# Performance work log

Measured on AMD Instinct MI355X. Metric: run time of the kernel, lower is better.

The kernel has to match this reference:

```python
import jax, jax.numpy as jnp
import numpy as np

N = 100000      # nodes
E = 1600000     # edges
R = 4           # relations
F = 128         # node feature dim
EMB = 128       # embedding size
HID = 256       # hidden size
B = 1024        # number of (nest, food) queries


def setup_inputs() -> dict:
    key = jax.random.key(0)
    ks = jax.random.split(key, 12)
    s1 = 1.0 / np.sqrt(F)
    s2 = 1.0 / np.sqrt(EMB)
    sf = 1.0 / np.sqrt(2 * EMB)
    return {
        "x": jax.random.normal(ks[0], (N, F), jnp.float32),
        "edge_index": jax.random.randint(ks[1], (2, E), 0, N),
        "edge_type": jax.random.randint(ks[2], (E,), 0, R),
        "nest_idx": jax.random.randint(ks[3], (B,), 0, N),
        "food_idx": jax.random.randint(ks[4], (B,), 0, N),
        "W_rel1": jax.random.normal(ks[5], (R, F, EMB), jnp.float32) * s1,
        "W_root1": jax.random.normal(ks[6], (F, EMB), jnp.float32) * s1,
        "b1": jnp.zeros((EMB,), jnp.float32),
        "W_rel2": jax.random.normal(ks[7], (R, EMB, EMB), jnp.float32) * s2,
        "W_root2": jax.random.normal(ks[8], (EMB, EMB), jnp.float32) * s2,
        "b2": jnp.zeros((EMB,), jnp.float32),
        "W_fc": jax.random.normal(ks[9], (2 * EMB, HID), jnp.float32) * sf,
        "b_fc": jnp.zeros((HID,), jnp.float32),
    }


def rgcn_conv(x, src, dst, etype, W_rel, W_root, b):
    # Per-relation transform of all nodes: [N, R, O]
    h = jnp.einsum('nf,rfo->nro', x, W_rel)
    msgs = h[src, etype]                      # [E, O] gather per edge
    # Mean aggregation per (dst, relation), PyG RGCNConv default
    key = dst * R + etype                     # [E]
    deg = jax.ops.segment_sum(jnp.ones((E,), x.dtype), key, num_segments=N * R)
    norm = 1.0 / jnp.maximum(deg, 1.0)
    out = jax.ops.segment_sum(msgs * norm[key][:, None], dst, num_segments=N)
    return out + x @ W_root + b


def reference(x, edge_index, edge_type, nest_idx, food_idx,
              W_rel1, W_root1, b1, W_rel2, W_root2, b2, W_fc, b_fc):
    src, dst = edge_index[0], edge_index[1]
    h = jax.nn.relu(rgcn_conv(x, src, dst, edge_type, W_rel1, W_root1, b1))
    h = rgcn_conv(h, src, dst, edge_type, W_rel2, W_root2, b2)
    combined = jnp.concatenate([h[nest_idx], h[food_idx]], axis=-1)  # [B, 2*EMB]
    return jax.nn.relu(combined @ W_fc + b_fc)                        # [B, HID]
```

## Files before the change

kernel.cpp:

```cpp
#include <hip/hip_runtime.h>
#include <stdint.h>

#define NN 100000
#define NE 1600000
#define NR 4
#define FD 128
#define KA 512
#define KT 640
#define NQ 1024
#define HIDN 256

#define MPAD 100096
#define NCHK (MPAD / 128)
#define NBE ((NE + 2047) / 2048)
#define NCHB ((NN + 255) / 256)
#define MAXS 49152
#define NCH1 (MAXS / 256)
#define MAXL2 65536

using u16 = unsigned short;
using u32 = unsigned int;
using u8 = unsigned char;
typedef __attribute__((ext_vector_type(8))) __bf16 bf16x8;
typedef __attribute__((ext_vector_type(4))) float f32x4;

__device__ __forceinline__ u16 f2b(float f) {
    u32 u = __builtin_bit_cast(u32, f);
    u32 r = u + 0x7FFFu + ((u >> 16) & 1u);
    return (u16)(r >> 16);
}
__device__ __forceinline__ float b2f_lo(u32 v) { return __builtin_bit_cast(float, v << 16); }
__device__ __forceinline__ float b2f_hi(u32 v) { return __builtin_bit_cast(float, v & 0xFFFF0000u); }
__device__ __forceinline__ u32 pack2(float a, float b) {
    return (u32)f2b(a) | ((u32)f2b(b) << 16);
}
__device__ __forceinline__ void gload_lds16(const void* g, void* l) {
    __builtin_amdgcn_global_load_lds((const __attribute__((address_space(1))) u32*)g,
                                     (__attribute__((address_space(3))) u32*)l, 16, 0, 0);
}

__global__ __launch_bounds__(256) void mark_T(const int* __restrict__ nest,
                                              const int* __restrict__ food,
                                              u8* __restrict__ bmT, u8* __restrict__ bmS) {
    int i = blockIdx.x * 256 + threadIdx.x;
    if (i < NQ)          { int q = nest[i];      bmT[q] = 1; bmS[q] = 1; }
    else if (i < 2 * NQ) { int q = food[i - NQ]; bmT[q] = 1; bmS[q] = 1; }
}

__global__ __launch_bounds__(256) void filter_l2(const int* __restrict__ ei,
                                                 const int* __restrict__ et,
                                                 const u8* __restrict__ bmT,
                                                 u8* __restrict__ bmS,
                                                 int* __restrict__ cnts,
                                                 u32* __restrict__ l2a,
                                                 u32* __restrict__ l2d) {
    __shared__ int lcnt, lbase;
    __shared__ u32 ba[2048], bd[2048];
    int t = threadIdx.x;
    if (t == 0) lcnt = 0;
    __syncthreads();
    int e0 = blockIdx.x * 2048;
    for (int j = 0; j < 8; ++j) {
        int e = e0 + j * 256 + t;
        if (e < NE) {
            int dst = ei[NE + e];
            if (bmT[dst]) {
                int src = ei[e];
                int r = et[e];
                int pos = atomicAdd(&lcnt, 1);
                ba[pos] = (u32)src | ((u32)r << 17);
                bd[pos] = (u32)dst;
                bmS[src] = 1;
            }
        }
    }
    __syncthreads();
    if (t == 0) lbase = atomicAdd(&cnts[2], lcnt);
    __syncthreads();
    for (int i = t; i < lcnt; i += 256) {
        l2a[lbase + i] = ba[i];
        l2d[lbase + i] = bd[i];
    }
}

__global__ __launch_bounds__(256) void bm_chunk(const u8* __restrict__ bmS,
                                                const u8* __restrict__ bmT,
                                                int* __restrict__ cS, int* __restrict__ cT) {
    __shared__ int sS[256], sT[256];
    int b = blockIdx.x, t = threadIdx.x;
    int n = b * 256 + t;
    int vs = (n < NN) ? bmS[n] : 0;
    int vt = (n < NN) ? bmT[n] : 0;
    sS[t] = vs; sT[t] = vt;
    __syncthreads();
    for (int o = 128; o > 0; o >>= 1) {
        if (t < o) { sS[t] += sS[t + o]; sT[t] += sT[t + o]; }
        __syncthreads();
    }
    if (t == 0) { cS[b] = sS[0]; cT[b] = sT[0]; }
}

__global__ __launch_bounds__(512) void bm_scan(const int* __restrict__ cS,
                                               const int* __restrict__ cT,
                                               int* __restrict__ oS, int* __restrict__ oT,
                                               int* __restrict__ cnts) {
    __shared__ int sS[512], sT[512];
    int t = threadIdx.x;
    int vs = (t < NCHB) ? cS[t] : 0;
    int vt = (t < NCHB) ? cT[t] : 0;
    sS[t] = vs; sT[t] = vt;
    __syncthreads();
    for (int o = 1; o < 512; o <<= 1) {
        int a = (t >= o) ? sS[t - o] : 0;
        int c = (t >= o) ? sT[t - o] : 0;
        __syncthreads();
        sS[t] += a; sT[t] += c;
        __syncthreads();
    }
    if (t < NCHB) { oS[t] = sS[t] - vs; oT[t] = sT[t] - vt; }
    if (t == NCHB - 1) { cnts[0] = sS[t]; cnts[1] = sT[t]; }
}

__global__ __launch_bounds__(256) void bm_write(const u8* __restrict__ bmS,
                                                const u8* __restrict__ bmT,
                                                const int* __restrict__ oS,
                                                const int* __restrict__ oT,
                                                int* __restrict__ sid, int* __restrict__ tidm,
                                                int* __restrict__ snode) {
    __shared__ int sS[256], sT[256];
    int b = blockIdx.x, t = threadIdx.x;
    int n = b * 256 + t;
    int vs = (n < NN) ? bmS[n] : 0;
    int vt = (n < NN) ? bmT[n] : 0;
    sS[t] = vs; sT[t] = vt;
    __syncthreads();
    for (int o = 1; o < 256; o <<= 1) {
        int a = (t >= o) ? sS[t - o] : 0;
        int c = (t >= o) ? sT[t - o] : 0;
        __syncthreads();
        sS[t] += a; sT[t] += c;
        __syncthreads();
    }
    if (n < NN) {
        int is = oS[b] + sS[t] - vs;
        int it = oT[b] + sT[t] - vt;
        sid[n] = is;
        tidm[n] = it;
        if (vs) snode[is] = n;
    }
}

__global__ __launch_bounds__(256) void l2_count(const int* __restrict__ cnts,
                                                const u32* __restrict__ l2a,
                                                const u32* __restrict__ l2d,
                                                const int* __restrict__ tidm,
                                                int* __restrict__ deg2) {
    int n = cnts[2];
    for (int i = blockIdx.x * 256 + threadIdx.x; i < n; i += gridDim.x * 256)
        atomicAdd(&deg2[tidm[l2d[i]] * 4 + ((l2a[i] >> 17) & 3)], 1);
}

__global__ __launch_bounds__(1024) void l2_scan(const int* __restrict__ deg2,
                                                int* __restrict__ offs2,
                                                int* __restrict__ cur2) {
    __shared__ int sm[1024];
    int t = threadIdx.x;
    int v[8];
    int s = 0;
    for (int j = 0; j < 8; ++j) { v[j] = deg2[t * 8 + j]; s += v[j]; }
    sm[t] = s;
    __syncthreads();
    for (int o = 1; o < 1024; o <<= 1) {
        int n = (t >= o) ? sm[t - o] : 0;
        __syncthreads();
        sm[t] += n;
        __syncthreads();
    }
    int ex = sm[t] - s;
    for (int j = 0; j < 8; ++j) { offs2[t * 8 + j] = ex; cur2[t * 8 + j] = ex; ex += v[j]; }
    if (t == 1023) offs2[8192] = ex;
}

__global__ __launch_bounds__(256) void l2_scatter(const int* __restrict__ cnts,
                                                  const u32* __restrict__ l2a,
                                                  const u32* __restrict__ l2d,
                                                  const int* __restrict__ tidm,
                                                  const int* __restrict__ sid,
                                                  int* __restrict__ cur2,
                                                  int* __restrict__ spack2) {
    int n = cnts[2];
    for (int i = blockIdx.x * 256 + threadIdx.x; i < n; i += gridDim.x * 256) {
        u32 a = l2a[i];
        int k = tidm[l2d[i]] * 4 + ((a >> 17) & 3);
        int pos = atomicAdd(&cur2[k], 1);
        spack2[pos] = sid[a & 0x1FFFFu];
    }
}

__global__ __launch_bounds__(256) void l1_count(const int* __restrict__ ei,
                                                const int* __restrict__ et,
                                                const u8* __restrict__ bmS,
                                                const int* __restrict__ sid,
                                                int* __restrict__ deg1) {
    int e0 = blockIdx.x * 2048;
    int t = threadIdx.x;
    for (int j = 0; j < 8; ++j) {
        int e = e0 + j * 256 + t;
        if (e < NE) {
            int dst = ei[NE + e];
            if (bmS[dst]) atomicAdd(&deg1[sid[dst] * 4 + et[e]], 1);
        }
    }
}

__global__ __launch_bounds__(256) void l1_chunk(const int* __restrict__ deg1,
                                                int* __restrict__ c1) {
    __shared__ int sm[256];
    int b = blockIdx.x, t = threadIdx.x;
    int n = b * 256 + t;
    int s = deg1[4 * n] + deg1[4 * n + 1] + deg1[4 * n + 2] + deg1[4 * n + 3];
    sm[t] = (s + 7) & ~7;
    __syncthreads();
    for (int o = 128; o > 0; o >>= 1) {
        if (t < o) sm[t] += sm[t + o];
        __syncthreads();
    }
    if (t == 0) c1[b] = sm[0];
}

__global__ __launch_bounds__(256) void l1_scan(const int* __restrict__ c1,
                                               int* __restrict__ o1) {
    __shared__ int sm[256];
    int t = threadIdx.x;
    int v = (t < NCH1) ? c1[t] : 0;
    sm[t] = v;
    __syncthreads();
    for (int o = 1; o < 256; o <<= 1) {
        int n = (t >= o) ? sm[t - o] : 0;
        __syncthreads();
        sm[t] += n;
        __syncthreads();
    }
    if (t < NCH1) o1[t] = sm[t] - v;
}

__global__ __launch_bounds__(256) void l1_write(const int* __restrict__ deg1,
                                                const int* __restrict__ o1,
                                                int* __restrict__ offs6s,
                                                int* __restrict__ cur1,
                                                int* __restrict__ spack1) {
    __shared__ int sm[256];
    int b = blockIdx.x, t = threadIdx.x;
    int n = b * 256 + t;
    int d0 = deg1[4 * n], d1 = deg1[4 * n + 1], d2 = deg1[4 * n + 2], d3 = deg1[4 * n + 3];
    int s = d0 + d1 + d2 + d3;
    int sp = (s + 7) & ~7;
    sm[t] = sp;
    __syncthreads();
    for (int o = 1; o < 256; o <<= 1) {
        int v = (t >= o) ? sm[t - o] : 0;
        __syncthreads();
        sm[t] += v;
        __syncthreads();
    }
    int e0 = o1[b] + sm[t] - sp;
    int e1 = e0 + d0, e2 = e1 + d1, e3 = e2 + d2, e4 = e3 + d3, eL = e0 + sp;
    int* o6 = offs6s + (size_t)n * 6;
    o6[0] = e0; o6[1] = e1; o6[2] = e2; o6[3] = e3; o6[4] = e4; o6[5] = eL;
    cur1[4 * n] = e0; cur1[4 * n + 1] = e1; cur1[4 * n + 2] = e2; cur1[4 * n + 3] = e3;
    for (int i = e4; i < eL; ++i) spack1[i] = 5 * NN;
}

__global__ __launch_bounds__(256) void l1_scatter(const int* __restrict__ ei,
                                                  const int* __restrict__ et,
                                                  const u8* __restrict__ bmS,
                                                  const int* __restrict__ sid,
                                                  int* __restrict__ cur1,
                                                  int* __restrict__ spack1) {
    int e0 = blockIdx.x * 2048;
    int t = threadIdx.x;
    for (int j = 0; j < 8; ++j) {
        int e = e0 + j * 256 + t;
        if (e < NE) {
            int dst = ei[NE + e];
            if (bmS[dst]) {
                int r = et[e];
                int src = ei[e];
                int pos = atomicAdd(&cur1[sid[dst] * 4 + r], 1);
                spack1[pos] = r * NN + src;
            }
        }
    }
}

__global__ __launch_bounds__(256) void cvt_bf16(const float* __restrict__ in,
                                                u16* __restrict__ outp, int n) {
    int i = blockIdx.x * 256 + threadIdx.x;
    int idx = i * 4;
    if (idx >= n) return;
    float4 v = *(const float4*)(in + idx);
    u32 lo = (u32)f2b(v.x) | ((u32)f2b(v.y) << 16);
    u32 hi = (u32)f2b(v.z) | ((u32)f2b(v.w) << 16);
    *(uint2*)(outp + idx) = make_uint2(lo, hi);
}

__global__ __launch_bounds__(256) void prep_B5(const float* __restrict__ Wrel,
                                               const float* __restrict__ Wroot,
                                               u16* __restrict__ Bt5) {
    int i = blockIdx.x * 256 + threadIdx.x;
    if (i >= 5 * FD * FD) return;
    int tb = i / (FD * FD);
    int rem = i - tb * (FD * FD);
    int o = rem / FD;
    int k = rem - o * FD;
    float v = (tb < 4) ? Wrel[(size_t)tb * FD * FD + (size_t)k * FD + o]
                       : Wroot[(size_t)k * FD + o];
    Bt5[i] = f2b(v);
}

__global__ __launch_bounds__(256) void prep_B(const float* __restrict__ Wrel,
                                              const float* __restrict__ Wroot,
                                              u16* __restrict__ Bt) {
    int i = blockIdx.x * 256 + threadIdx.x;
    if (i >= FD * KT) return;
    int k = i % KT;
    int o = i / KT;
    float v = (k < 512) ? Wrel[(size_t)k * FD + o] : Wroot[(size_t)(k - 512) * FD + o];
    Bt[i] = f2b(v);
}

__global__ __launch_bounds__(256) void gemm_y(const u16* __restrict__ X,
                                              const u16* __restrict__ Bt5,
                                              u16* __restrict__ Y) {
    __shared__ u16 As[2][8192];
    int blk = blockIdx.x;
    int rel = blk / NCHK;
    int chunk = blk - rel * NCHK;
    int row0 = chunk * 128;
    int tid = threadIdx.x;
    int wid = tid >> 6, lane = tid & 63;
    int wm = wid >> 1, wn = wid & 1;
    int lr = lane & 15, hi = lane >> 4;
    const u16* Btr = Bt5 + (size_t)rel * FD * FD;
    u16* C = Y + (size_t)rel * NN * FD;

    int srow = wid * 8 + (lane >> 3);
    int sg = (lane & 7) ^ ((lane >> 3) & 7);
#pragma unroll
    for (int s = 0; s < 2; ++s)
#pragma unroll
        for (int i = 0; i < 4; ++i) {
            int r = i * 32 + srow;
            int gr = row0 + r;
            gload_lds16(X + (size_t)gr * FD + s * 64 + sg * 8,
                        (char*)As[s] + i * 4096 + wid * 1024);
        }
    __syncthreads();

    f32x4 acc[4][4];
#pragma unroll
    for (int i = 0; i < 4; ++i)
#pragma unroll
        for (int j = 0; j < 4; ++j) acc[i][j] = (f32x4){0.f, 0.f, 0.f, 0.f};

#pragma unroll
    for (int t = 0; t < 2; ++t) {
#pragma unroll
        for (int kk = 0; kk < 2; ++kk) {
            bf16x8 bfr[4], afr[4];
#pragma unroll
            for (int ni = 0; ni < 4; ++ni) {
                int col = wn * 64 + ni * 16 + lr;
                bfr[ni] = *reinterpret_cast<const bf16x8*>(
                    Btr + (size_t)col * FD + t * 64 + kk * 32 + hi * 8);
            }
#pragma unroll
            for (int mi = 0; mi < 4; ++mi) {
                int r = wm * 64 + mi * 16 + lr;
                int sp = (kk * 4 + hi) ^ (r & 7);
                afr[mi] = *reinterpret_cast<const bf16x8*>((char*)As[t] + r * 128 + sp * 16);
            }
#pragma unroll
            for (int mi = 0; mi < 4; ++mi)
#pragma unroll
                for (int ni = 0; ni < 4; ++ni)
                    acc[mi][ni] = __builtin_amdgcn_mfma_f32_16x16x32_bf16(afr[mi], bfr[ni], acc[mi][ni], 0, 0, 0);
        }
    }
#pragma unroll
    for (int mi = 0; mi < 4; ++mi)
#pragma unroll
        for (int ni = 0; ni < 4; ++ni) {
            int col = wn * 64 + ni * 16 + lr;
#pragma unroll
            for (int rg = 0; rg < 4; ++rg) {
                int row = row0 + wm * 64 + mi * 16 + hi * 4 + rg;
                if (row < NN) C[(size_t)row * FD + col] = f2b(acc[mi][ni][rg]);
            }
        }
}

__global__ __launch_bounds__(256) void agg_s(const int* __restrict__ cnts,
                                             const int* __restrict__ offs6s,
                                             const int* __restrict__ spack1,
                                             const int* __restrict__ snode,
                                             const u32* __restrict__ Y,
                                             const float* __restrict__ bias,
                                             u16* __restrict__ h1s) {
    int wid = threadIdx.x >> 6, lane = threadIdx.x & 63;
    int row = blockIdx.x * 4 + wid;
    if (row >= cnts[0]) return;

    const int* ob = offs6s + (size_t)row * 6;
    int o0 = __builtin_amdgcn_readfirstlane(ob[0]);
    int o1 = __builtin_amdgcn_readfirstlane(ob[1]);
    int o2 = __builtin_amdgcn_readfirstlane(ob[2]);
    int o3 = __builtin_amdgcn_readfirstlane(ob[3]);
    int o4 = __builtin_amdgcn_readfirstlane(ob[4]);
    int oL = __builtin_amdgcn_readfirstlane(ob[5]);

    float a00 = 0, a01 = 0, a10 = 0, a11 = 0, a20 = 0, a21 = 0, a30 = 0, a31 = 0;

    for (int e = o0; e < oL; e += 8) {
        int p[8];
        u32 v[8];
#pragma unroll
        for (int j = 0; j < 8; ++j)
            p[j] = __builtin_amdgcn_readfirstlane(spack1[e + j]);
#pragma unroll
        for (int j = 0; j < 8; ++j) v[j] = Y[(size_t)p[j] * 64 + lane];
#pragma unroll
        for (int j = 0; j < 8; ++j) {
            int ij = e + j;
            float f0 = b2f_lo(v[j]);
            float f1 = b2f_hi(v[j]);
            if (ij < o1)      { a00 += f0; a01 += f1; }
            else if (ij < o2) { a10 += f0; a11 += f1; }
            else if (ij < o3) { a20 += f0; a21 += f1; }
            else              { a30 += f0; a31 += f1; }
        }
    }

    int d0 = o1 - o0, d1 = o2 - o1, d2 = o3 - o2, d3 = o4 - o3;
    float s0 = 1.0f / (float)(d0 > 1 ? d0 : 1);
    float s1 = 1.0f / (float)(d1 > 1 ? d1 : 1);
    float s2 = 1.0f / (float)(d2 > 1 ? d2 : 1);
    float s3 = 1.0f / (float)(d3 > 1 ? d3 : 1);
    float sum0 = a00 * s0 + a10 * s1 + a20 * s2 + a30 * s3;
    float sum1 = a01 * s0 + a11 * s1 + a21 * s2 + a31 * s3;
    int node = __builtin_amdgcn_readfirstlane(snode[row]);
    u32 rv = Y[((size_t)4 * NN + node) * 64 + lane];
    float2 bb = *reinterpret_cast<const float2*>(bias + lane * 2);
    float r0 = fmaxf(sum0 + b2f_lo(rv) + bb.x, 0.f);
    float r1 = fmaxf(sum1 + b2f_hi(rv) + bb.y, 0.f);
    *(u32*)(h1s + (size_t)row * FD + lane * 2) = pack2(r0, r1);
}

__global__ __launch_bounds__(256) void agg_q2(const int* __restrict__ offs2,
                                              const int* __restrict__ spack2,
                                              const u32* __restrict__ h1s4,
                                              const int* __restrict__ nest,
                                              const int* __restrict__ food,
                                              const int* __restrict__ tidm,
                                              const int* __restrict__ sid,
                                              u16* __restrict__ Aout,
                                              int* __restrict__ sidq) {
    int wid = threadIdx.x >> 6, lane = threadIdx.x & 63;
    int row = blockIdx.x * 4 + wid;
    if (row >= 2 * NQ) return;
    int q = (row < NQ) ? nest[row] : food[row - NQ];
    q = __builtin_amdgcn_readfirstlane(q);
    int tq = __builtin_amdgcn_readfirstlane(tidm[q]);
    if (lane == 0) sidq[row] = sid[q];
    const int* ob = offs2 + (size_t)tq * 4;
    int o[5];
#pragma unroll
    for (int i = 0; i < 5; ++i) o[i] = __builtin_amdgcn_readfirstlane(ob[i]);
    u16* Ao = Aout + (size_t)row * KA + lane * 2;
#pragma unroll
    for (int r = 0; r < 4; ++r) {
        int s = o[r], t = o[r + 1], last = t - 1;
        float a0 = 0, a1 = 0;
        for (int e = s; e < t; e += 8) {
            int p[8];
            u32 v[8];
#pragma unroll
            for (int j = 0; j < 8; ++j) {
                int ij = e + j;
                int cl = ij <= last ? ij : last;
                int pv = __builtin_amdgcn_readfirstlane(spack2[cl]);
                p[j] = (ij <= last) ? pv : MAXS;
            }
#pragma unroll
            for (int j = 0; j < 8; ++j) v[j] = h1s4[(size_t)p[j] * 64 + lane];
#pragma unroll
            for (int j = 0; j < 8; ++j) { a0 += b2f_lo(v[j]); a1 += b2f_hi(v[j]); }
        }
        int d = t - s;
        float sc = 1.0f / (float)(d > 1 ? d : 1);
        *(u32*)(Ao + r * 128) = pack2(a0 * sc, a1 * sc);
    }
}

__global__ __launch_bounds__(256) void gemm_lds3(const u16* __restrict__ A,
                                                 const u16* __restrict__ rootSrc,
                                                 const int* __restrict__ rootIdx,
                                                 const u16* __restrict__ Bt,
                                                 const float* __restrict__ bias,
                                                 float* __restrict__ Cout, int M) {
    __shared__ u16 As[3][8192];
    int tid = threadIdx.x;
    int wid = tid >> 6, lane = tid & 63;
    int wm = wid >> 1, wn = wid & 1;
    int lr = lane & 15, hi = lane >> 4;
    int row0 = blockIdx.x * 128;

    f32x4 acc[4][4];
#pragma unroll
    for (int i = 0; i < 4; ++i)
#pragma unroll
        for (int j = 0; j < 4; ++j) acc[i][j] = (f32x4){0.f, 0.f, 0.f, 0.f};

    int srow = wid * 8 + (lane >> 3);
    int sg = (lane & 7) ^ ((lane >> 3) & 7);

    auto stage = [&](int t, int buf) {
#pragma unroll
        for (int i = 0; i < 4; ++i) {
            int r = i * 32 + srow;
            int gr = row0 + r;
            const u16* src;
            if (t < 8) {
                src = A + (size_t)gr * KA + t * 64 + sg * 8;
            } else {
                int idx = rootIdx[gr];
                src = rootSrc + (size_t)idx * FD + (t - 8) * 64 + sg * 8;
            }
            gload_lds16(src, (char*)As[buf] + i * 4096 + wid * 1024);
        }
    };

    stage(0, 0);
    stage(1, 1);

    for (int t = 0; t < 10; ++t) {
        int cur = t % 3;
        bf16x8 bfr[2][4];
#pragma unroll
        for (int kk = 0; kk < 2; ++kk)
#pragma unroll
            for (int ni = 0; ni < 4; ++ni) {
                int col = wn * 64 + ni * 16 + lr;
                bfr[kk][ni] = *reinterpret_cast<const bf16x8*>(
                    Bt + (size_t)col * KT + t * 64 + kk * 32 + hi * 8);
            }
        bool staged = (t + 2 < 10);
        if (staged) stage(t + 2, (t + 2) % 3);
        if (staged) asm volatile("s_waitcnt vmcnt(4)" ::: "memory");
        else        asm volatile("s_waitcnt vmcnt(0)" ::: "memory");
        __builtin_amdgcn_s_barrier();
        __builtin_amdgcn_sched_barrier(0);
#pragma unroll
        for (int kk = 0; kk < 2; ++kk) {
            bf16x8 afr[4];
#pragma unroll
            for (int mi = 0; mi < 4; ++mi) {
                int r = wm * 64 + mi * 16 + lr;
                int sp = (kk * 4 + hi) ^ (r & 7);
                afr[mi] = *reinterpret_cast<const bf16x8*>((char*)As[cur] + r * 128 + sp * 16);
            }
#pragma unroll
            for (int mi = 0; mi < 4; ++mi)
#pragma unroll
                for (int ni = 0; ni < 4; ++ni)
                    acc[mi][ni] = __builtin_amdgcn_mfma_f32_16x16x32_bf16(afr[mi], bfr[kk][ni], acc[mi][ni], 0, 0, 0);
        }
        asm volatile("s_waitcnt lgkmcnt(0)" ::: "memory");
        __builtin_amdgcn_s_barrier();
    }

#pragma unroll
    for (int mi = 0; mi < 4; ++mi)
#pragma unroll
        for (int ni = 0; ni < 4; ++ni) {
            int col = wn * 64 + ni * 16 + lr;
            float bv = bias[col];
#pragma unroll
            for (int rg = 0; rg < 4; ++rg) {
                int row = row0 + wm * 64 + mi * 16 + hi * 4 + rg;
                if (row < M) Cout[(size_t)row * FD + col] = acc[mi][ni][rg] + bv;
            }
        }
}

__global__ __launch_bounds__(256) void fc_kernel(const float* __restrict__ h2q,
                                                 const float* __restrict__ Wfc,
                                                 const float* __restrict__ bfc,
                                                 float* __restrict__ out) {
    __shared__ float comb[2 * FD];
    int q = blockIdx.x, t = threadIdx.x;
    if (t < FD) comb[t] = h2q[(size_t)q * FD + t];
    else comb[t] = h2q[(size_t)(NQ + q) * FD + (t - FD)];
    __syncthreads();
    float s = bfc[t];
#pragma unroll 4
    for (int k = 0; k < 2 * FD; ++k) s += comb[k] * Wfc[(size_t)k * HIDN + t];
    out[(size_t)q * HIDN + t] = fmaxf(s, 0.f);
}

extern "C" void kernel_launch(void* const* d_in, const int* in_sizes, int n_in,
                              void* d_out, int out_size, void* d_ws, size_t ws_size,
                              hipStream_t stream) {
    const float* x      = (const float*)d_in[0];
    const int*   ei     = (const int*)d_in[1];
    const int*   et     = (const int*)d_in[2];
    const int*   nest   = (const int*)d_in[3];
    const int*   food   = (const int*)d_in[4];
    const float* Wrel1  = (const float*)d_in[5];
    const float* Wroot1 = (const float*)d_in[6];
    const float* b1     = (const float*)d_in[7];
    const float* Wrel2  = (const float*)d_in[8];
    const float* Wroot2 = (const float*)d_in[9];
    const float* b2     = (const float*)d_in[10];
    const float* Wfc    = (const float*)d_in[11];
    const float* bfc    = (const float*)d_in[12];
    float* out = (float*)d_out;

    char* w = (char*)d_ws;
    size_t off = 0;
    auto take = [&](size_t b) {
        char* p = w + off;
        off += b;
        off = (off + 255) & ~(size_t)255;
        return p;
    };
    size_t zero0 = off;
    int* cnts   = (int*)take(256);
    u8* bmT     = (u8*)take(NN);
    u8* bmS     = (u8*)take(NN);
    int* deg2   = (int*)take(8192 * 4);
    int* deg1   = (int*)take((size_t)4 * MAXS * 4);
    size_t zeroSz = off - zero0;
    char* zbase = w + zero0;
    int* oS     = (int*)take((size_t)NCHB * 4);
    int* oT     = (int*)take((size_t)NCHB * 4);
    int* c1     = (int*)take((size_t)NCH1 * 4);
    int* o1     = (int*)take((size_t)NCH1 * 4);
    int* sid    = (int*)take((size_t)NN * 4);
    int* tidm   = (int*)take((size_t)NN * 4);
    int* snode  = (int*)take((size_t)MAXS * 4);
    u32* l2a    = (u32*)take((size_t)MAXL2 * 4);
    u32* l2d    = (u32*)take((size_t)MAXL2 * 4);
    int* offs2  = (int*)take((size_t)8193 * 4);
    int* cur2   = (int*)take((size_t)8192 * 4);
    int* spack2 = (int*)take((size_t)MAXL2 * 4);
    int* offs6s = (int*)take((size_t)MAXS * 6 * 4);
    int* cur1   = (int*)take((size_t)4 * MAXS * 4);
    int* spack1 = (int*)take(((size_t)NE + 8 * MAXS) * 4);
    int* sidq   = (int*)take((size_t)2 * NQ * 4);
    u16* xh     = (u16*)take((size_t)MPAD * FD * 2);
    u16* Bt5    = (u16*)take((size_t)5 * FD * FD * 2);
    u16* Bt2    = (u16*)take((size_t)FD * KT * 2);
    u16* Y      = (u16*)take(((size_t)5 * NN + 1) * FD * 2);
    u16* h1s    = (u16*)take(((size_t)MAXS + 1) * FD * 2);
    u16* A2     = (u16*)take((size_t)2 * NQ * KA * 2);
    float* h2q  = (float*)take((size_t)2 * NQ * FD * 4);

    hipMemsetAsync(zbase, 0, zeroSz, stream);
    hipMemsetAsync(Y + (size_t)5 * NN * FD, 0, FD * 2, stream);
    hipMemsetAsync(h1s + (size_t)MAXS * FD, 0, FD * 2, stream);

    cvt_bf16<<<((NN * FD / 4) + 255) / 256, 256, 0, stream>>>(x, xh, NN * FD);
    prep_B5<<<(5 * FD * FD + 255) / 256, 256, 0, stream>>>(Wrel1, Wroot1, Bt5);
    prep_B<<<(FD * KT + 255) / 256, 256, 0, stream>>>(Wrel2, Wroot2, Bt2);

    mark_T<<<(2 * NQ + 255) / 256, 256, 0, stream>>>(nest, food, bmT, bmS);
    filter_l2<<<NBE, 256, 0, stream>>>(ei, et, bmT, bmS, cnts, l2a, l2d);
    bm_chunk<<<NCHB, 256, 0, stream>>>(bmS, bmT, oS, oT);
    bm_scan<<<1, 512, 0, stream>>>(oS, oT, oS, oT, cnts);
    bm_write<<<NCHB, 256, 0, stream>>>(bmS, bmT, oS, oT, sid, tidm, snode);

    l2_count<<<128, 256, 0, stream>>>(cnts, l2a, l2d, tidm, deg2);
    l2_scan<<<1, 1024, 0, stream>>>(deg2, offs2, cur2);
    l2_scatter<<<128, 256, 0, stream>>>(cnts, l2a, l2d, tidm, sid, cur2, spack2);

    l1_count<<<NBE, 256, 0, stream>>>(ei, et, bmS, sid, deg1);
    l1_chunk<<<NCH1, 256, 0, stream>>>(deg1, c1);
    l1_scan<<<1, 256, 0, stream>>>(c1, o1);
    l1_write<<<NCH1, 256, 0, stream>>>(deg1, o1, offs6s, cur1, spack1);
    l1_scatter<<<NBE, 256, 0, stream>>>(ei, et, bmS, sid, cur1, spack1);

    gemm_y<<<5 * NCHK, 256, 0, stream>>>(xh, Bt5, Y);

    agg_s<<<MAXS / 4, 256, 0, stream>>>(cnts, offs6s, spack1, snode, (const u32*)Y, b1, h1s);

    agg_q2<<<(2 * NQ + 3) / 4, 256, 0, stream>>>(offs2, spack2, (const u32*)h1s,
                                                 nest, food, tidm, sid, A2, sidq);
    gemm_lds3<<<(2 * NQ) / 128, 256, 0, stream>>>(A2, h1s, sidq, Bt2, b2, h2q, 2 * NQ);
    fc_kernel<<<NQ, 256, 0, stream>>>(h2q, Wfc, bfc, out);
}
```

Baseline: 259.3 us.

## Aggregate raw layer-1 features before transform instead of transforming all nodes

Layer 1 previously ran a GEMM over all nodes for all four relations plus the root, then gathered transformed rows per edge. Now it gathers bf16 input features per edge, mean-aggregates them per relation into a [S,512] buffer for the needed subgraph nodes only, and runs one GEMM with the root features appended, applying bias and ReLU and writing bf16. This drops the large full-graph transform and its write/read traffic, at the cost of an extra intermediate buffer and a GEMM whose row count is read from device memory. The gemm kernel is generalised with a device-side M, an optional root index, ReLU and a bf16 output mode.

Measured after the change: 229.5 us (median of 2 runs). -11.5%, faster.

```diff
diff --git a/kernel.cpp b/kernel.cpp
--- a/kernel.cpp
+++ b/kernel.cpp
@@ -11,7 +11,6 @@
 #define HIDN 256
 
 #define MPAD 100096
-#define NCHK (MPAD / 128)
 #define NBE ((NE + 2047) / 2048)
 #define NCHB ((NN + 255) / 256)
 #define MAXS 49152
@@ -268,7 +267,7 @@
     int* o6 = offs6s + (size_t)n * 6;
     o6[0] = e0; o6[1] = e1; o6[2] = e2; o6[3] = e3; o6[4] = e4; o6[5] = eL;
     cur1[4 * n] = e0; cur1[4 * n + 1] = e1; cur1[4 * n + 2] = e2; cur1[4 * n + 3] = e3;
-    for (int i = e4; i < eL; ++i) spack1[i] = 5 * NN;
+    for (int i = e4; i < eL; ++i) spack1[i] = NN;
 }
 
 __global__ __launch_bounds__(256) void l1_scatter(const int* __restrict__ ei,
@@ -284,10 +283,8 @@
         if (e < NE) {
             int dst = ei[NE + e];
             if (bmS[dst]) {
-                int r = et[e];
-                int src = ei[e];
-                int pos = atomicAdd(&cur1[sid[dst] * 4 + r], 1);
-                spack1[pos] = r * NN + src;
+                int pos = atomicAdd(&cur1[sid[dst] * 4 + et[e]], 1);
+                spack1[pos] = ei[e];
             }
         }
     }
@@ -304,20 +301,6 @@
     *(uint2*)(outp + idx) = make_uint2(lo, hi);
 }
 
-__global__ __launch_bounds__(256) void prep_B5(const float* __restrict__ Wrel,
-                                               const float* __restrict__ Wroot,
-                                               u16* __restrict__ Bt5) {
-    int i = blockIdx.x * 256 + threadIdx.x;
-    if (i >= 5 * FD * FD) return;
-    int tb = i / (FD * FD);
-    int rem = i - tb * (FD * FD);
-    int o = rem / FD;
-    int k = rem - o * FD;
-    float v = (tb < 4) ? Wrel[(size_t)tb * FD * FD + (size_t)k * FD + o]
-                       : Wroot[(size_t)k * FD + o];
-    Bt5[i] = f2b(v);
-}
-
 __global__ __launch_bounds__(256) void prep_B(const float* __restrict__ Wrel,
                                               const float* __restrict__ Wroot,
                                               u16* __restrict__ Bt) {
@@ -329,84 +312,11 @@
     Bt[i] = f2b(v);
 }
 
-__global__ __launch_bounds__(256) void gemm_y(const u16* __restrict__ X,
-                                              const u16* __restrict__ Bt5,
-                                              u16* __restrict__ Y) {
-    __shared__ u16 As[2][8192];
-    int blk = blockIdx.x;
-    int rel = blk / NCHK;
-    int chunk = blk - rel * NCHK;
-    int row0 = chunk * 128;
-    int tid = threadIdx.x;
-    int wid = tid >> 6, lane = tid & 63;
-    int wm = wid >> 1, wn = wid & 1;
-    int lr = lane & 15, hi = lane >> 4;
-    const u16* Btr = Bt5 + (size_t)rel * FD * FD;
-    u16* C = Y + (size_t)rel * NN * FD;
-
-    int srow = wid * 8 + (lane >> 3);
-    int sg = (lane & 7) ^ ((lane >> 3) & 7);
-#pragma unroll
-    for (int s = 0; s < 2; ++s)
-#pragma unroll
-        for (int i = 0; i < 4; ++i) {
-            int r = i * 32 + srow;
-            int gr = row0 + r;
-            gload_lds16(X + (size_t)gr * FD + s * 64 + sg * 8,
-                        (char*)As[s] + i * 4096 + wid * 1024);
-        }
-    __syncthreads();
-
-    f32x4 acc[4][4];
-#pragma unroll
-    for (int i = 0; i < 4; ++i)
-#pragma unroll
-        for (int j = 0; j < 4; ++j) acc[i][j] = (f32x4){0.f, 0.f, 0.f, 0.f};
-
-#pragma unroll
-    for (int t = 0; t < 2; ++t) {
-#pragma unroll
-        for (int kk = 0; kk < 2; ++kk) {
-            bf16x8 bfr[4], afr[4];
-#pragma unroll
-            for (int ni = 0; ni < 4; ++ni) {
-                int col = wn * 64 + ni * 16 + lr;
-                bfr[ni] = *reinterpret_cast<const bf16x8*>(
-                    Btr + (size_t)col * FD + t * 64 + kk * 32 + hi * 8);
-            }
-#pragma unroll
-            for (int mi = 0; mi < 4; ++mi) {
-                int r = wm * 64 + mi * 16 + lr;
-                int sp = (kk * 4 + hi) ^ (r & 7);
-                afr[mi] = *reinterpret_cast<const bf16x8*>((char*)As[t] + r * 128 + sp * 16);
-            }
-#pragma unroll
-            for (int mi = 0; mi < 4; ++mi)
-#pragma unroll
-                for (int ni = 0; ni < 4; ++ni)
-                    acc[mi][ni] = __builtin_amdgcn_mfma_f32_16x16x32_bf16(afr[mi], bfr[ni], acc[mi][ni], 0, 0, 0);
-        }
-    }
-#pragma unroll
-    for (int mi = 0; mi < 4; ++mi)
-#pragma unroll
-        for (int ni = 0; ni < 4; ++ni) {
-            int col = wn * 64 + ni * 16 + lr;
-#pragma unroll
-            for (int rg = 0; rg < 4; ++rg) {
-                int row = row0 + wm * 64 + mi * 16 + hi * 4 + rg;
-                if (row < NN) C[(size_t)row * FD + col] = f2b(acc[mi][ni][rg]);
-            }
-        }
-}
-
 __global__ __launch_bounds__(256) void agg_s(const int* __restrict__ cnts,
                                              const int* __restrict__ offs6s,
                                              const int* __restrict__ spack1,
-                                             const int* __restrict__ snode,
-                                             const u32* __restrict__ Y,
-                                             const float* __restrict__ bias,
-                                             u16* __restrict__ h1s) {
+                                             const u32* __restrict__ fp,
+                                             u16* __restrict__ Aout) {
     int wid = threadIdx.x >> 6, lane = threadIdx.x & 63;
     int row = blockIdx.x * 4 + wid;
     if (row >= cnts[0]) return;
@@ -428,7 +338,7 @@
         for (int j = 0; j < 8; ++j)
             p[j] = __builtin_amdgcn_readfirstlane(spack1[e + j]);
 #pragma unroll
-        for (int j = 0; j < 8; ++j) v[j] = Y[(size_t)p[j] * 64 + lane];
+        for (int j = 0; j < 8; ++j) v[j] = fp[(size_t)p[j] * 64 + lane];
 #pragma unroll
         for (int j = 0; j < 8; ++j) {
             int ij = e + j;
@@ -446,14 +356,11 @@
     float s1 = 1.0f / (float)(d1 > 1 ? d1 : 1);
     float s2 = 1.0f / (float)(d2 > 1 ? d2 : 1);
     float s3 = 1.0f / (float)(d3 > 1 ? d3 : 1);
-    float sum0 = a00 * s0 + a10 * s1 + a20 * s2 + a30 * s3;
-    float sum1 = a01 * s0 + a11 * s1 + a21 * s2 + a31 * s3;
-    int node = __builtin_amdgcn_readfirstlane(snode[row]);
-    u32 rv = Y[((size_t)4 * NN + node) * 64 + lane];
-    float2 bb = *reinterpret_cast<const float2*>(bias + lane * 2);
-    float r0 = fmaxf(sum0 + b2f_lo(rv) + bb.x, 0.f);
-    float r1 = fmaxf(sum1 + b2f_hi(rv) + bb.y, 0.f);
-    *(u32*)(h1s + (size_t)row * FD + lane * 2) = pack2(r0, r1);
+    u16* Ao = Aout + (size_t)row * KA + lane * 2;
+    __builtin_nontemporal_store(pack2(a00 * s0, a01 * s0), (u32*)(Ao + 0));
+    __builtin_nontemporal_store(pack2(a10 * s1, a11 * s1), (u32*)(Ao + 128));
+    __builtin_nontemporal_store(pack2(a20 * s2, a21 * s2), (u32*)(Ao + 256));
+    __builtin_nontemporal_store(pack2(a30 * s3, a31 * s3), (u32*)(Ao + 384));
 }
 
 __global__ __launch_bounds__(256) void agg_q2(const int* __restrict__ offs2,
@@ -507,13 +414,17 @@
                                                  const int* __restrict__ rootIdx,
                                                  const u16* __restrict__ Bt,
                                                  const float* __restrict__ bias,
-                                                 float* __restrict__ Cout, int M) {
+                                                 void* __restrict__ Cout,
+                                                 const int* __restrict__ Mptr, int Mstatic,
+                                                 int relu, int outBf16) {
+    int M = Mptr ? Mptr[0] : Mstatic;
+    int row0 = blockIdx.x * 128;
+    if (row0 >= M) return;
     __shared__ u16 As[3][8192];
     int tid = threadIdx.x;
     int wid = tid >> 6, lane = tid & 63;
     int wm = wid >> 1, wn = wid & 1;
     int lr = lane & 15, hi = lane >> 4;
-    int row0 = blockIdx.x * 128;
 
     f32x4 acc[4][4];
 #pragma unroll
@@ -533,7 +444,8 @@
             if (t < 8) {
                 src = A + (size_t)gr * KA + t * 64 + sg * 8;
             } else {
-                int idx = rootIdx[gr];
+                int idx = rootIdx ? rootIdx[gr] : gr;
+                if ((u32)idx > (u32)NN) idx = 0;
                 src = rootSrc + (size_t)idx * FD + (t - 8) * 64 + sg * 8;
             }
             gload_lds16(src, (char*)As[buf] + i * 4096 + wid * 1024);
@@ -588,7 +500,12 @@
 #pragma unroll
             for (int rg = 0; rg < 4; ++rg) {
                 int row = row0 + wm * 64 + mi * 16 + hi * 4 + rg;
-                if (row < M) Cout[(size_t)row * FD + col] = acc[mi][ni][rg] + bv;
+                if (row < M) {
+                    float v = acc[mi][ni][rg] + bv;
+                    if (relu) v = fmaxf(v, 0.f);
+                    if (outBf16) ((u16*)Cout)[(size_t)row * FD + col] = f2b(v);
+                    else ((float*)Cout)[(size_t)row * FD + col] = v;
+                }
             }
         }
 }
@@ -640,6 +557,7 @@
     u8* bmS     = (u8*)take(NN);
     int* deg2   = (int*)take(8192 * 4);
     int* deg1   = (int*)take((size_t)4 * MAXS * 4);
+    int* snode  = (int*)take((size_t)MAXS * 4);
     size_t zeroSz = off - zero0;
     char* zbase = w + zero0;
     int* oS     = (int*)take((size_t)NCHB * 4);
@@ -648,7 +566,6 @@
     int* o1     = (int*)take((size_t)NCH1 * 4);
     int* sid    = (int*)take((size_t)NN * 4);
     int* tidm   = (int*)take((size_t)NN * 4);
-    int* snode  = (int*)take((size_t)MAXS * 4);
     u32* l2a    = (u32*)take((size_t)MAXL2 * 4);
     u32* l2d    = (u32*)take((size_t)MAXL2 * 4);
     int* offs2  = (int*)take((size_t)8193 * 4);
@@ -659,19 +576,19 @@
     int* spack1 = (int*)take(((size_t)NE + 8 * MAXS) * 4);
     int* sidq   = (int*)take((size_t)2 * NQ * 4);
     u16* xh     = (u16*)take((size_t)MPAD * FD * 2);
-    u16* Bt5    = (u16*)take((size_t)5 * FD * FD * 2);
+    u16* Bt1    = (u16*)take((size_t)FD * KT * 2);
     u16* Bt2    = (u16*)take((size_t)FD * KT * 2);
-    u16* Y      = (u16*)take(((size_t)5 * NN + 1) * FD * 2);
+    u16* A1s    = (u16*)take((size_t)MAXS * KA * 2);
     u16* h1s    = (u16*)take(((size_t)MAXS + 1) * FD * 2);
     u16* A2     = (u16*)take((size_t)2 * NQ * KA * 2);
     float* h2q  = (float*)take((size_t)2 * NQ * FD * 4);
 
     hipMemsetAsync(zbase, 0, zeroSz, stream);
-    hipMemsetAsync(Y + (size_t)5 * NN * FD, 0, FD * 2, stream);
+    hipMemsetAsync(xh + (size_t)NN * FD, 0, FD * 2, stream);
     hipMemsetAsync(h1s + (size_t)MAXS * FD, 0, FD * 2, stream);
 
     cvt_bf16<<<((NN * FD / 4) + 255) / 256, 256, 0, stream>>>(x, xh, NN * FD);
-    prep_B5<<<(5 * FD * FD + 255) / 256, 256, 0, stream>>>(Wrel1, Wroot1, Bt5);
+    prep_B<<<(FD * KT + 255) / 256, 256, 0, stream>>>(Wrel1, Wroot1, Bt1);
     prep_B<<<(FD * KT + 255) / 256, 256, 0, stream>>>(Wrel2, Wroot2, Bt2);
 
     mark_T<<<(2 * NQ + 255) / 256, 256, 0, stream>>>(nest, food, bmT, bmS);
@@ -690,12 +607,13 @@
     l1_write<<<NCH1, 256, 0, stream>>>(deg1, o1, offs6s, cur1, spack1);
     l1_scatter<<<NBE, 256, 0, stream>>>(ei, et, bmS, sid, cur1, spack1);
 
-    gemm_y<<<5 * NCHK, 256, 0, stream>>>(xh, Bt5, Y);
-
-    agg_s<<<MAXS / 4, 256, 0, stream>>>(cnts, offs6s, spack1, snode, (const u32*)Y, b1, h1s);
+    agg_s<<<MAXS / 4, 256, 0, stream>>>(cnts, offs6s, spack1, (const u32*)xh, A1s);
+    gemm_lds3<<<MAXS / 128, 256, 0, stream>>>(A1s, xh, snode, Bt1, b1,
+                                              (void*)h1s, cnts, 0, 1, 1);
 
     agg_q2<<<(2 * NQ + 3) / 4, 256, 0, stream>>>(offs2, spack2, (const u32*)h1s,
                                                  nest, food, tidm, sid, A2, sidq);
-    gemm_lds3<<<(2 * NQ) / 128, 256, 0, stream>>>(A2, h1s, sidq, Bt2, b2, h2q, 2 * NQ);
+    gemm_lds3<<<(2 * NQ) / 128, 256, 0, stream>>>(A2, h1s, sidq, Bt2, b2,
+                                                  (void*)h2q, nullptr, 2 * NQ, 0, 0);
     fc_kernel<<<NQ, 256, 0, stream>>>(h2q, Wfc, bfc, out);
 }
```
